# Optimization experiments

Hardware: AMD Instinct MI355X
Metric: run time of the kernel (lower is better)

The kernel has to match this reference:

```python
import jax, jax.numpy as jnp
import numpy as np

B, T, E, H = 2, 2048, 1024, 16
D = E // H  # head dim = 64
ROPE_BASE = 10000.0


def setup_inputs() -> dict:
    key = jax.random.key(0)
    k0, k1, k2 = jax.random.split(key, 3)
    s = 0.02  # GPT-style init scale
    return {
        "x": jax.random.normal(k0, (B, T, E), jnp.float32),
        "w_qkv": jax.random.normal(k1, (E, 3 * E), jnp.float32) * s,
        "b_qkv": jnp.zeros((3 * E,), jnp.float32),
        "w_out": jax.random.normal(k2, (E, E), jnp.float32) * s,
        "b_out": jnp.zeros((E,), jnp.float32),
    }


def _rope_tables(t, d, dtype):
    # Llama rotary with scale=1 (YaRN degenerates to vanilla RoPE)
    inv_freq = 1.0 / (ROPE_BASE ** (jnp.arange(0, d, 2, dtype=jnp.float32) / d))
    freqs = jnp.arange(t, dtype=jnp.float32)[:, None] * inv_freq[None, :]  # [T, D/2]
    emb = jnp.concatenate([freqs, freqs], axis=-1)  # [T, D]
    return jnp.cos(emb).astype(dtype), jnp.sin(emb).astype(dtype)


def _rotate_half(x):
    return jnp.concatenate([-x[..., D // 2:], x[..., : D // 2]], axis=-1)


def reference(x, w_qkv, b_qkv, w_out, b_out):
    # 1) fused QKV projection
    qkv = x @ w_qkv + b_qkv                      # [B, T, 3E]
    q, k, v = jnp.split(qkv, 3, axis=-1)

    def heads(t):
        return t.reshape(B, T, H, D).transpose(0, 2, 1, 3)  # [B, H, T, D]

    q, k, v = heads(q), heads(k), heads(v)

    # 2) rotary position embedding on q, k
    cos, sin = _rope_tables(T, D, x.dtype)       # [T, D], broadcasts over B, H
    q = q * cos + _rotate_half(q) * sin
    k = k * cos + _rotate_half(k) * sin

    # 3) causal scaled dot-product attention
    scale = jnp.asarray(1.0 / np.sqrt(D), x.dtype)
    scores = jnp.einsum("bhqd,bhkd->bhqk", q, k) * scale
    causal = jnp.tril(jnp.ones((T, T), dtype=bool))
    scores = jnp.where(causal, scores, jnp.finfo(scores.dtype).min)
    attn = jax.nn.softmax(scores, axis=-1)
    out = jnp.einsum("bhqk,bhkd->bhqd", attn, v)  # [B, H, T, D]

    # 4) merge heads + output projection
    out = out.transpose(0, 2, 1, 3).reshape(B, T, E)
    return out @ w_out + b_out
```

## Files before the change

kernel.cpp:

```cpp
#include <hip/hip_runtime.h>
#include <hip/hip_bf16.h>
#include <stdint.h>

#define B_  2
#define T_  2048
#define E_  1024
#define H_  16
#define D_  64
#define BH_ 32

typedef unsigned short ushort_t;
typedef __attribute__((ext_vector_type(8))) short bfrag;
typedef __attribute__((ext_vector_type(4))) short s16x4;
typedef __attribute__((ext_vector_type(4))) float f32x4;

__device__ __forceinline__ ushort_t f2b(float f) {
    uint32_t u = __builtin_bit_cast(uint32_t, f);
    u += 0x7fffu + ((u >> 16) & 1u);
    return (ushort_t)(u >> 16);
}
__device__ __forceinline__ float b2f(ushort_t h) {
    return __builtin_bit_cast(float, (uint32_t)h << 16);
}

#if defined(__has_builtin)
#if __has_builtin(__builtin_amdgcn_exp2f)
#define EXP2(x) __builtin_amdgcn_exp2f(x)
#endif
#endif
#ifndef EXP2
__device__ __forceinline__ float hexp2_(float x) {
    float r;
    asm volatile("v_exp_f32 %0, %1\n\ts_nop 1" : "=v"(r) : "v"(x));
    return r;
}
#define EXP2(x) hexp2_(x)
#endif

__device__ __forceinline__ uint32_t cvtpk_bf16(float lo, float hi) {
    uint32_t r;
    asm("v_cvt_pk_bf16_f32 %0, %1, %2" : "=v"(r) : "v"(lo), "v"(hi));
    return r;
}

typedef const __attribute__((address_space(1))) uint8_t* gas_t;
typedef __attribute__((address_space(3))) uint8_t* las_t;
__device__ __forceinline__ void gload_lds16(const void* g, void* l) {
    __builtin_amdgcn_global_load_lds((gas_t)g, (las_t)l, 16, 0, 0);
}

__global__ __launch_bounds__(256) void rope_table_kernel(float2* __restrict__ cs) {
    int id = blockIdx.x * 256 + threadIdx.x;
    int j = id & 31, t = id >> 5;
    float ang = (float)t * expf(-(float)j * 0.2878231366242558f);
    float s, c;
    sincosf(ang, &s, &c);
    cs[id] = make_float2(c, s);
}

__global__ __launch_bounds__(256) void cast_x_kernel(const float* __restrict__ in, ushort_t* __restrict__ out) {
    int i = (blockIdx.x * 256 + threadIdx.x) * 8;
    float4 a = *(const float4*)(in + i);
    float4 b = *(const float4*)(in + i + 4);
    ushort_t r[8] = {f2b(a.x), f2b(a.y), f2b(a.z), f2b(a.w), f2b(b.x), f2b(b.y), f2b(b.z), f2b(b.w)};
    *(uint4*)(out + i) = *(const uint4*)r;
}

__global__ __launch_bounds__(256) void transpose_cast_kernel(const float* __restrict__ in, ushort_t* __restrict__ out,
                                                             int R, int C) {
    __shared__ float tile[32][33];
    int tx = threadIdx.x, ty = threadIdx.y;
    int c0 = blockIdx.x * 32, r0 = blockIdx.y * 32;
#pragma unroll
    for (int i = 0; i < 4; ++i)
        tile[ty + i * 8][tx] = in[(size_t)(r0 + ty + i * 8) * C + c0 + tx];
    __syncthreads();
#pragma unroll
    for (int i = 0; i < 4; ++i)
        out[(size_t)(c0 + ty + i * 8) * R + r0 + tx] = f2b(tile[tx][ty + i * 8]);
}

__global__ __launch_bounds__(256) void gemm_qkv_kernel(const ushort_t* __restrict__ A, const ushort_t* __restrict__ Bt,
                                                       const float* __restrict__ bias, const float2* __restrict__ cstab,
                                                       ushort_t* __restrict__ qw, ushort_t* __restrict__ kw,
                                                       ushort_t* __restrict__ vw) {
    const int K = 1024;
    __shared__ ushort_t As[128 * 64];
    __shared__ ushort_t Bs[128 * 64];
    int tid = threadIdx.x, lane = tid & 63, wid = tid >> 6;
    int lm = lane & 15, lg = lane >> 4;
    int bid = blockIdx.x;
    int xcd = bid & 7, idx = bid >> 3;
    int bm = xcd * 4 + idx / 24;
    int bn = idx % 24;
    int wm = wid >> 1, wn = wid & 1;

    int cbase = bn * 128 + wn * 64;
    bool qk = (cbase < 2048);

    f32x4 acc[4][4] = {};
    const ushort_t* ag = A + (size_t)bm * 128 * K;
    const ushort_t* bg = Bt + (size_t)bn * 128 * K;

    for (int kt = 0; kt < K / 64; ++kt) {
        __syncthreads();
#pragma unroll
        for (int c = 0; c < 4; ++c) {
            int G = c * 256 + tid;
            int rr = G >> 3;
            int gs = (G & 7) ^ (rr & 7);
            gload_lds16(ag + (size_t)rr * K + kt * 64 + gs * 8, As + (c * 256 + wid * 64) * 8);
            gload_lds16(bg + (size_t)rr * K + kt * 64 + gs * 8, Bs + (c * 256 + wid * 64) * 8);
        }
        __syncthreads();
        bfrag a[2][4], b[2][4];
#pragma unroll
        for (int kk = 0; kk < 2; ++kk) {
#pragma unroll
            for (int mi = 0; mi < 4; ++mi) {
                int row = wm * 64 + mi * 16 + lm;
                int slot = (kk * 4 + lg) ^ (lm & 7);
                a[kk][mi] = *(const bfrag*)&As[row * 64 + slot * 8];
            }
#pragma unroll
            for (int ni = 0; ni < 4; ++ni) {
                int row = wn * 64 + ni * 16 + lm;
                int slot = (kk * 4 + lg) ^ (lm & 7);
                b[kk][ni] = *(const bfrag*)&Bs[row * 64 + slot * 8];
            }
        }
        if (qk) {
#pragma unroll
            for (int kk = 0; kk < 2; ++kk)
#pragma unroll
                for (int mi = 0; mi < 4; ++mi)
#pragma unroll
                    for (int ni = 0; ni < 4; ++ni)
                        acc[mi][ni] = __builtin_amdgcn_mfma_f32_16x16x32_bf16(b[kk][ni], a[kk][mi], acc[mi][ni], 0, 0, 0);
        } else {
#pragma unroll
            for (int kk = 0; kk < 2; ++kk)
#pragma unroll
                for (int mi = 0; mi < 4; ++mi)
#pragma unroll
                    for (int ni = 0; ni < 4; ++ni)
                        acc[mi][ni] = __builtin_amdgcn_mfma_f32_16x16x32_bf16(a[kk][mi], b[kk][ni], acc[mi][ni], 0, 0, 0);
        }
    }

    int sel = cbase >> 10;
    int h = (cbase & 1023) >> 6;
    if (qk) {
        ushort_t* dst = sel ? kw : qw;
        float scale = sel ? 1.0f : 0.18033688011112042f;
        float4 bias4[4];
#pragma unroll
        for (int ni = 0; ni < 4; ++ni)
            bias4[ni] = *(const float4*)&bias[cbase + ni * 16 + lg * 4];
#pragma unroll
        for (int mi = 0; mi < 4; ++mi) {
            int r = bm * 128 + wm * 64 + mi * 16 + lm;
            int bb = r >> 11, t = r & (T_ - 1);
            size_t rowbase = ((size_t)(bb * H_ + h) * T_ + t) * D_;
            const float4* csrow = (const float4*)(cstab + t * 32);
#pragma unroll
            for (int nip = 0; nip < 2; ++nip) {
                float4 ca = csrow[nip * 4 + lg];
                float4 cb = csrow[nip * 4 + lg + 2 * (nip == 0 ? 1 : 1) - 1];
                const float4* cs2 = (const float4*)(cstab + t * 32 + nip * 16 + lg * 4);
                ca = cs2[0]; cb = cs2[1];
                float xl[4], xh[4];
#pragma unroll
                for (int i = 0; i < 4; ++i) {
                    xl[i] = acc[mi][nip][i]     + ((const float*)&bias4[nip])[i];
                    xh[i] = acc[mi][nip + 2][i] + ((const float*)&bias4[nip + 2])[i];
                }
                float c0 = ca.x, s0 = ca.y, c1 = ca.z, s1 = ca.w;
                float c2 = cb.x, s2 = cb.y, c3 = cb.z, s3 = cb.w;
                float rl0 = (xl[0] * c0 - xh[0] * s0) * scale;
                float rl1 = (xl[1] * c1 - xh[1] * s1) * scale;
                float rl2 = (xl[2] * c2 - xh[2] * s2) * scale;
                float rl3 = (xl[3] * c3 - xh[3] * s3) * scale;
                float rh0 = (xh[0] * c0 + xl[0] * s0) * scale;
                float rh1 = (xh[1] * c1 + xl[1] * s1) * scale;
                float rh2 = (xh[2] * c2 + xl[2] * s2) * scale;
                float rh3 = (xh[3] * c3 + xl[3] * s3) * scale;
                uint2 wlo, whi;
                wlo.x = cvtpk_bf16(rl0, rl1); wlo.y = cvtpk_bf16(rl2, rl3);
                whi.x = cvtpk_bf16(rh0, rh1); whi.y = cvtpk_bf16(rh2, rh3);
                *(uint2*)&dst[rowbase + nip * 16 + lg * 4]      = wlo;
                *(uint2*)&dst[rowbase + 32 + nip * 16 + lg * 4] = whi;
            }
        }
    } else {
        float bb4[4];
#pragma unroll
        for (int ni = 0; ni < 4; ++ni) bb4[ni] = bias[cbase + ni * 16 + lm];
#pragma unroll
        for (int ni = 0; ni < 4; ++ni) {
            int d = ni * 16 + lm;
#pragma unroll
            for (int mi = 0; mi < 4; ++mi) {
                int r = bm * 128 + wm * 64 + mi * 16 + lg * 4;
                int bb = r >> 11, tq = r & (T_ - 1);
                uint2 w;
                w.x = cvtpk_bf16(acc[mi][ni][0] + bb4[ni], acc[mi][ni][1] + bb4[ni]);
                w.y = cvtpk_bf16(acc[mi][ni][2] + bb4[ni], acc[mi][ni][3] + bb4[ni]);
                *(uint2*)&vw[((size_t)(bb * H_ + h) * D_ + d) * T_ + tq] = w;
            }
        }
    }
}

__device__ __forceinline__ void stage_tile(const ushort_t* __restrict__ kb, const ushort_t* __restrict__ vb,
                                           ushort_t* kdst, ushort_t* vdst, int k0, int wid, int lane) {
#pragma unroll
    for (int c = 0; c < 2; ++c) {
        int G = (c * 4 + wid) * 64 + lane;
        int rr = G >> 3;
        int gs = (G & 7) ^ (rr & 7);
        gload_lds16(kb + (size_t)(k0 + rr) * D_ + gs * 8, kdst + (c * 4 + wid) * 512);
        gload_lds16(vb + (size_t)rr * T_ + k0 + gs * 8, vdst + (c * 4 + wid) * 512);
    }
}

__global__ __launch_bounds__(256, 2) void flash_kernel(const ushort_t* __restrict__ q, const ushort_t* __restrict__ k,
                                                       const ushort_t* __restrict__ vt, ushort_t* __restrict__ o) {
    __shared__ ushort_t smem[2][4096];
    int tid = threadIdx.x, lane = tid & 63, wid = tid >> 6;
    int lm = lane & 15, lg = lane >> 4;
    int x = blockIdx.x & 7, r = blockIdx.x >> 3;
    int half = r >> 5, idx = r & 31;
    int bh = x * 4 + (idx & 3);
    int jq = idx >> 2;
    int j = half ? jq : 15 - jq;
    int q0w = j * 128 + wid * 32;
    int b = bh >> 4, h = bh & 15;
    int nt = 2 * j + 2;

    const ushort_t* qb = q + (size_t)bh * T_ * D_;
    const ushort_t* kb = k + (size_t)bh * T_ * D_;
    const ushort_t* vb = vt + (size_t)bh * D_ * T_;

    bfrag aq[2][2];
#pragma unroll
    for (int s = 0; s < 2; ++s)
#pragma unroll
        for (int hh = 0; hh < 2; ++hh)
            aq[s][hh] = *(const bfrag*)(qb + (size_t)(q0w + s * 16 + lm) * D_ + hh * 32 + lg * 8);

    f32x4 acc[2][4] = {};
    float lsum[2] = {0.f, 0.f};

    for (int t = 0; t < nt; ++t) {
        int k0 = t * 64;
        __syncthreads();
        stage_tile(kb, vb, smem[0], smem[1], k0, wid, lane);
        asm volatile("s_waitcnt vmcnt(0)" ::: "memory");
        __builtin_amdgcn_sched_barrier(0);
        __syncthreads();

        if (k0 <= q0w + 31) {
            bfrag ka[4][2];
#pragma unroll
            for (int sb = 0; sb < 4; ++sb)
#pragma unroll
                for (int hh = 0; hh < 2; ++hh) {
                    int rr = sb * 16 + lm;
                    int gr = (hh * 4 + lg) ^ (rr & 7);
                    ka[sb][hh] = *(const bfrag*)&smem[0][rr * 64 + gr * 8];
                }
            s16x4 vq[4][4];
#pragma unroll
            for (int qq = 0; qq < 4; ++qq)
#pragma unroll
                for (int db = 0; db < 4; ++db) {
                    int rr = db * 16 + lm;
                    int gr = (qq * 2 + (lg >> 1)) ^ (rr & 7);
                    vq[qq][db] = *(const s16x4*)&smem[1][rr * 64 + gr * 8 + (lg & 1) * 4];
                }
            f32x4 st[2][4];
#pragma unroll
            for (int s = 0; s < 2; ++s)
#pragma unroll
                for (int sb = 0; sb < 4; ++sb) {
                    f32x4 z = {};
                    z = __builtin_amdgcn_mfma_f32_16x16x32_bf16(ka[sb][0], aq[s][0], z, 0, 0, 0);
                    st[s][sb] = __builtin_amdgcn_mfma_f32_16x16x32_bf16(ka[sb][1], aq[s][1], z, 0, 0, 0);
                }
            if (k0 + 63 > q0w) {
#pragma unroll
                for (int s = 0; s < 2; ++s)
#pragma unroll
                    for (int sb = 0; sb < 4; ++sb)
#pragma unroll
                        for (int i = 0; i < 4; ++i)
                            if (k0 + sb * 16 + lg * 4 + i > q0w + s * 16 + lm) st[s][sb][i] = -1e30f;
            }
#pragma unroll
            for (int s = 0; s < 2; ++s) {
                float pv[4][4];
#pragma unroll
                for (int sb = 0; sb < 4; ++sb)
#pragma unroll
                    for (int i = 0; i < 4; ++i)
                        pv[sb][i] = EXP2(st[s][sb][i]);
                lsum[s] += ((pv[0][0] + pv[0][1]) + (pv[0][2] + pv[0][3])) +
                           ((pv[1][0] + pv[1][1]) + (pv[1][2] + pv[1][3])) +
                           ((pv[2][0] + pv[2][1]) + (pv[2][2] + pv[2][3])) +
                           ((pv[3][0] + pv[3][1]) + (pv[3][2] + pv[3][3]));
                uint4 u0, u1;
                u0.x = cvtpk_bf16(pv[0][0], pv[0][1]);
                u0.y = cvtpk_bf16(pv[0][2], pv[0][3]);
                u0.z = cvtpk_bf16(pv[1][0], pv[1][1]);
                u0.w = cvtpk_bf16(pv[1][2], pv[1][3]);
                u1.x = cvtpk_bf16(pv[2][0], pv[2][1]);
                u1.y = cvtpk_bf16(pv[2][2], pv[2][3]);
                u1.z = cvtpk_bf16(pv[3][0], pv[3][1]);
                u1.w = cvtpk_bf16(pv[3][2], pv[3][3]);
                bfrag pf0 = __builtin_bit_cast(bfrag, u0);
                bfrag pf1 = __builtin_bit_cast(bfrag, u1);
#pragma unroll
                for (int db = 0; db < 4; ++db) {
                    bfrag va01 = __builtin_shufflevector(vq[0][db], vq[1][db], 0, 1, 2, 3, 4, 5, 6, 7);
                    bfrag va23 = __builtin_shufflevector(vq[2][db], vq[3][db], 0, 1, 2, 3, 4, 5, 6, 7);
                    acc[s][db] = __builtin_amdgcn_mfma_f32_16x16x32_bf16(va01, pf0, acc[s][db], 0, 0, 0);
                    acc[s][db] = __builtin_amdgcn_mfma_f32_16x16x32_bf16(va23, pf1, acc[s][db], 0, 0, 0);
                }
            }
        }
    }

#pragma unroll
    for (int s = 0; s < 2; ++s) {
        float lM = lsum[s];
        lM += __shfl_xor(lM, 16);
        lM += __shfl_xor(lM, 32);
        float inv = 1.0f / lM;
        int tq = q0w + s * 16 + lm;
        size_t ro = ((size_t)b * T_ + tq) * E_ + h * D_;
#pragma unroll
        for (int db = 0; db < 4; ++db) {
            uint2 w;
            w.x = cvtpk_bf16(acc[s][db][0] * inv, acc[s][db][1] * inv);
            w.y = cvtpk_bf16(acc[s][db][2] * inv, acc[s][db][3] * inv);
            *(uint2*)(o + ro + db * 16 + lg * 4) = w;
        }
    }
}

__global__ __launch_bounds__(256) void gemm_out_kernel(const ushort_t* __restrict__ A, const ushort_t* __restrict__ Bt,
                                                       const float* __restrict__ bias, float* __restrict__ out) {
    const int K = 1024;
    __shared__ ushort_t As[128 * 64];
    __shared__ ushort_t Bs[64 * 64];
    int tid = threadIdx.x, lane = tid & 63, wid = tid >> 6;
    int lm = lane & 15, lg = lane >> 4;
    int bid = blockIdx.x;
    int xcd = bid & 7, idx = bid >> 3;
    int bm = xcd * 4 + idx / 16;
    int bn = idx % 16;

    f32x4 acc[2][4] = {};
    const ushort_t* ag = A + (size_t)bm * 128 * K;
    const ushort_t* bg = Bt + (size_t)bn * 64 * K;

    for (int kt = 0; kt < K / 64; ++kt) {
        __syncthreads();
#pragma unroll
        for (int c = 0; c < 4; ++c) {
            int G = c * 256 + tid;
            int rr = G >> 3;
            int gs = (G & 7) ^ (rr & 7);
            gload_lds16(ag + (size_t)rr * K + kt * 64 + gs * 8, As + (c * 256 + wid * 64) * 8);
        }
#pragma unroll
        for (int c = 0; c < 2; ++c) {
            int G = c * 256 + tid;
            int rr = G >> 3;
            int gs = (G & 7) ^ (rr & 7);
            gload_lds16(bg + (size_t)rr * K + kt * 64 + gs * 8, Bs + (c * 256 + wid * 64) * 8);
        }
        __syncthreads();
        bfrag a[2][2], b[2][4];
#pragma unroll
        for (int kk = 0; kk < 2; ++kk) {
#pragma unroll
            for (int mi = 0; mi < 2; ++mi) {
                int row = wid * 32 + mi * 16 + lm;
                int slot = (kk * 4 + lg) ^ (lm & 7);
                a[kk][mi] = *(const bfrag*)&As[row * 64 + slot * 8];
            }
#pragma unroll
            for (int ni = 0; ni < 4; ++ni) {
                int row = ni * 16 + lm;
                int slot = (kk * 4 + lg) ^ (lm & 7);
                b[kk][ni] = *(const bfrag*)&Bs[row * 64 + slot * 8];
            }
        }
#pragma unroll
        for (int kk = 0; kk < 2; ++kk)
#pragma unroll
            for (int mi = 0; mi < 2; ++mi)
#pragma unroll
                for (int ni = 0; ni < 4; ++ni)
                    acc[mi][ni] = __builtin_amdgcn_mfma_f32_16x16x32_bf16(a[kk][mi], b[kk][ni], acc[mi][ni], 0, 0, 0);
    }
#pragma unroll
    for (int ni = 0; ni < 4; ++ni) {
        int c = bn * 64 + ni * 16 + lm;
        float bb = bias[c];
#pragma unroll
        for (int mi = 0; mi < 2; ++mi) {
#pragma unroll
            for (int i = 0; i < 4; ++i) {
                int r = bm * 128 + wid * 32 + mi * 16 + lg * 4 + i;
                out[(size_t)r * 1024 + c] = acc[mi][ni][i] + bb;
            }
        }
    }
}

extern "C" void kernel_launch(void* const* d_in, const int* in_sizes, int n_in,
                              void* d_out, int out_size, void* d_ws, size_t ws_size,
                              hipStream_t stream) {
    const float* x     = (const float*)d_in[0];
    const float* w_qkv = (const float*)d_in[1];
    const float* b_qkv = (const float*)d_in[2];
    const float* w_out = (const float*)d_in[3];
    const float* b_out = (const float*)d_in[4];
    float* out = (float*)d_out;

    ushort_t* ws    = (ushort_t*)d_ws;
    ushort_t* xb    = ws;
    ushort_t* wqkvT = xb + 4194304;
    ushort_t* woutT = wqkvT + 3145728;
    ushort_t* qw    = woutT + 1048576;
    ushort_t* kw    = qw + 4194304;
    ushort_t* vw    = kw + 4194304;
    ushort_t* ao    = vw + 4194304;
    float2*   cstab = (float2*)(ao + 4194304);

    rope_table_kernel<<<256, 256, 0, stream>>>(cstab);
    cast_x_kernel<<<2048, 256, 0, stream>>>(x, xb);
    transpose_cast_kernel<<<dim3(96, 32), dim3(32, 8), 0, stream>>>(w_qkv, wqkvT, 1024, 3072);
    transpose_cast_kernel<<<dim3(32, 32), dim3(32, 8), 0, stream>>>(w_out, woutT, 1024, 1024);
    gemm_qkv_kernel<<<dim3(768), 256, 0, stream>>>(xb, wqkvT, b_qkv, cstab, qw, kw, vw);
    flash_kernel<<<dim3(512), 256, 0, stream>>>(qw, kw, vw, ao);
    gemm_out_kernel<<<dim3(512), 256, 0, stream>>>(ao, woutT, b_out, out);
}
```

Before: 118.8 us.

## Double-buffer LDS in both GEMMs and merge prep kernels into one launch

Both the QKV and output-projection GEMMs now use two LDS buffers: the global-to-LDS load for the next K tile is issued before the MFMAs on the current tile, so load latency overlaps compute and each iteration has one barrier instead of two. The four preprocessing kernels (rope table, x cast, two weight transposes) are merged into one launch that dispatches on block index, removing three kernel launches. The cost is doubled LDS use per block (64KB for the QKV GEMM), which may lower occupancy, and the prep kernel is now a single block-heterogeneous grid. The RoPE epilogue gets a small cleanup of redundant loads.

```diff
diff --git a/kernel.cpp b/kernel.cpp
--- a/kernel.cpp
+++ b/kernel.cpp
@@ -18,9 +18,6 @@
     uint32_t u = __builtin_bit_cast(uint32_t, f);
     u += 0x7fffu + ((u >> 16) & 1u);
     return (ushort_t)(u >> 16);
-}
-__device__ __forceinline__ float b2f(ushort_t h) {
-    return __builtin_bit_cast(float, (uint32_t)h << 16);
 }
 
 #if defined(__has_builtin)
@@ -48,36 +45,46 @@
 __device__ __forceinline__ void gload_lds16(const void* g, void* l) {
     __builtin_amdgcn_global_load_lds((gas_t)g, (las_t)l, 16, 0, 0);
 }
-
-__global__ __launch_bounds__(256) void rope_table_kernel(float2* __restrict__ cs) {
-    int id = blockIdx.x * 256 + threadIdx.x;
-    int j = id & 31, t = id >> 5;
-    float ang = (float)t * expf(-(float)j * 0.2878231366242558f);
-    float s, c;
-    sincosf(ang, &s, &c);
-    cs[id] = make_float2(c, s);
-}
-
-__global__ __launch_bounds__(256) void cast_x_kernel(const float* __restrict__ in, ushort_t* __restrict__ out) {
-    int i = (blockIdx.x * 256 + threadIdx.x) * 8;
-    float4 a = *(const float4*)(in + i);
-    float4 b = *(const float4*)(in + i + 4);
-    ushort_t r[8] = {f2b(a.x), f2b(a.y), f2b(a.z), f2b(a.w), f2b(b.x), f2b(b.y), f2b(b.z), f2b(b.w)};
-    *(uint4*)(out + i) = *(const uint4*)r;
-}
-
-__global__ __launch_bounds__(256) void transpose_cast_kernel(const float* __restrict__ in, ushort_t* __restrict__ out,
-                                                             int R, int C) {
+__device__ __forceinline__ void drain_vmem() {
+    asm volatile("s_waitcnt vmcnt(0)" ::: "memory");
+    __builtin_amdgcn_sched_barrier(0);
+}
+
+__global__ __launch_bounds__(256) void prep_kernel(const float* __restrict__ x, const float* __restrict__ w_qkv,
+                                                   const float* __restrict__ w_out, ushort_t* __restrict__ xb,
+                                                   ushort_t* __restrict__ wqkvT, ushort_t* __restrict__ woutT,
+                                                   float2* __restrict__ cstab) {
     __shared__ float tile[32][33];
-    int tx = threadIdx.x, ty = threadIdx.y;
-    int c0 = blockIdx.x * 32, r0 = blockIdx.y * 32;
-#pragma unroll
-    for (int i = 0; i < 4; ++i)
-        tile[ty + i * 8][tx] = in[(size_t)(r0 + ty + i * 8) * C + c0 + tx];
-    __syncthreads();
-#pragma unroll
-    for (int i = 0; i < 4; ++i)
-        out[(size_t)(c0 + ty + i * 8) * R + r0 + tx] = f2b(tile[tx][ty + i * 8]);
+    int blk = blockIdx.x, tid = threadIdx.x;
+    if (blk < 256) {
+        int id = blk * 256 + tid;
+        int j = id & 31, t = id >> 5;
+        float ang = (float)t * expf(-(float)j * 0.2878231366242558f);
+        float s, c;
+        sincosf(ang, &s, &c);
+        cstab[id] = make_float2(c, s);
+    } else if (blk < 2304) {
+        int i = ((blk - 256) * 256 + tid) * 8;
+        float4 a = *(const float4*)(x + i);
+        float4 b = *(const float4*)(x + i + 4);
+        ushort_t r[8] = {f2b(a.x), f2b(a.y), f2b(a.z), f2b(a.w), f2b(b.x), f2b(b.y), f2b(b.z), f2b(b.w)};
+        *(uint4*)(xb + i) = *(const uint4*)r;
+    } else {
+        const float* in;
+        ushort_t* out;
+        int R, C, bx, by;
+        if (blk < 5376) { in = w_qkv; out = wqkvT; R = 1024; C = 3072; int t = blk - 2304; bx = t % 96; by = t / 96; }
+        else            { in = w_out; out = woutT; R = 1024; C = 1024; int t = blk - 5376; bx = t % 32; by = t / 32; }
+        int tx = tid & 31, ty = tid >> 5;
+        int c0 = bx * 32, r0 = by * 32;
+#pragma unroll
+        for (int i = 0; i < 4; ++i)
+            tile[ty + i * 8][tx] = in[(size_t)(r0 + ty + i * 8) * C + c0 + tx];
+        __syncthreads();
+#pragma unroll
+        for (int i = 0; i < 4; ++i)
+            out[(size_t)(c0 + ty + i * 8) * R + r0 + tx] = f2b(tile[tx][ty + i * 8]);
+    }
 }
 
 __global__ __launch_bounds__(256) void gemm_qkv_kernel(const ushort_t* __restrict__ A, const ushort_t* __restrict__ Bt,
@@ -85,8 +92,8 @@
                                                        ushort_t* __restrict__ qw, ushort_t* __restrict__ kw,
                                                        ushort_t* __restrict__ vw) {
     const int K = 1024;
-    __shared__ ushort_t As[128 * 64];
-    __shared__ ushort_t Bs[128 * 64];
+    __shared__ ushort_t As[2][128 * 64];
+    __shared__ ushort_t Bs[2][128 * 64];
     int tid = threadIdx.x, lane = tid & 63, wid = tid >> 6;
     int lm = lane & 15, lg = lane >> 4;
     int bid = blockIdx.x;
@@ -102,17 +109,23 @@
     const ushort_t* ag = A + (size_t)bm * 128 * K;
     const ushort_t* bg = Bt + (size_t)bn * 128 * K;
 
+#define QKV_STAGE(kt_, buf_)                                                              \
+    _Pragma("unroll")                                                                     \
+    for (int c = 0; c < 4; ++c) {                                                         \
+        int G = c * 256 + tid;                                                            \
+        int rr = G >> 3;                                                                  \
+        int gs = (G & 7) ^ (rr & 7);                                                      \
+        gload_lds16(ag + (size_t)rr * K + (kt_) * 64 + gs * 8, &As[buf_][(c * 256 + wid * 64) * 8]); \
+        gload_lds16(bg + (size_t)rr * K + (kt_) * 64 + gs * 8, &Bs[buf_][(c * 256 + wid * 64) * 8]); \
+    }
+
+    int cur = 0;
+    QKV_STAGE(0, 0);
+    drain_vmem();
+    __syncthreads();
+
     for (int kt = 0; kt < K / 64; ++kt) {
-        __syncthreads();
-#pragma unroll
-        for (int c = 0; c < 4; ++c) {
-            int G = c * 256 + tid;
-            int rr = G >> 3;
-            int gs = (G & 7) ^ (rr & 7);
-            gload_lds16(ag + (size_t)rr * K + kt * 64 + gs * 8, As + (c * 256 + wid * 64) * 8);
-            gload_lds16(bg + (size_t)rr * K + kt * 64 + gs * 8, Bs + (c * 256 + wid * 64) * 8);
-        }
-        __syncthreads();
+        if (kt + 1 < K / 64) { QKV_STAGE(kt + 1, cur ^ 1); }
         bfrag a[2][4], b[2][4];
 #pragma unroll
         for (int kk = 0; kk < 2; ++kk) {
@@ -120,13 +133,13 @@
             for (int mi = 0; mi < 4; ++mi) {
                 int row = wm * 64 + mi * 16 + lm;
                 int slot = (kk * 4 + lg) ^ (lm & 7);
-                a[kk][mi] = *(const bfrag*)&As[row * 64 + slot * 8];
+                a[kk][mi] = *(const bfrag*)&As[cur][row * 64 + slot * 8];
             }
 #pragma unroll
             for (int ni = 0; ni < 4; ++ni) {
                 int row = wn * 64 + ni * 16 + lm;
                 int slot = (kk * 4 + lg) ^ (lm & 7);
-                b[kk][ni] = *(const bfrag*)&Bs[row * 64 + slot * 8];
+                b[kk][ni] = *(const bfrag*)&Bs[cur][row * 64 + slot * 8];
             }
         }
         if (qk) {
@@ -146,7 +159,11 @@
                     for (int ni = 0; ni < 4; ++ni)
                         acc[mi][ni] = __builtin_amdgcn_mfma_f32_16x16x32_bf16(a[kk][mi], b[kk][ni], acc[mi][ni], 0, 0, 0);
         }
-    }
+        drain_vmem();
+        __syncthreads();
+        cur ^= 1;
+    }
+#undef QKV_STAGE
 
     int sel = cbase >> 10;
     int h = (cbase & 1023) >> 6;
@@ -162,29 +179,24 @@
             int r = bm * 128 + wm * 64 + mi * 16 + lm;
             int bb = r >> 11, t = r & (T_ - 1);
             size_t rowbase = ((size_t)(bb * H_ + h) * T_ + t) * D_;
-            const float4* csrow = (const float4*)(cstab + t * 32);
 #pragma unroll
             for (int nip = 0; nip < 2; ++nip) {
-                float4 ca = csrow[nip * 4 + lg];
-                float4 cb = csrow[nip * 4 + lg + 2 * (nip == 0 ? 1 : 1) - 1];
                 const float4* cs2 = (const float4*)(cstab + t * 32 + nip * 16 + lg * 4);
-                ca = cs2[0]; cb = cs2[1];
+                float4 ca = cs2[0], cb = cs2[1];
                 float xl[4], xh[4];
 #pragma unroll
                 for (int i = 0; i < 4; ++i) {
                     xl[i] = acc[mi][nip][i]     + ((const float*)&bias4[nip])[i];
                     xh[i] = acc[mi][nip + 2][i] + ((const float*)&bias4[nip + 2])[i];
                 }
-                float c0 = ca.x, s0 = ca.y, c1 = ca.z, s1 = ca.w;
-                float c2 = cb.x, s2 = cb.y, c3 = cb.z, s3 = cb.w;
-                float rl0 = (xl[0] * c0 - xh[0] * s0) * scale;
-                float rl1 = (xl[1] * c1 - xh[1] * s1) * scale;
-                float rl2 = (xl[2] * c2 - xh[2] * s2) * scale;
-                float rl3 = (xl[3] * c3 - xh[3] * s3) * scale;
-                float rh0 = (xh[0] * c0 + xl[0] * s0) * scale;
-                float rh1 = (xh[1] * c1 + xl[1] * s1) * scale;
-                float rh2 = (xh[2] * c2 + xl[2] * s2) * scale;
-                float rh3 = (xh[3] * c3 + xl[3] * s3) * scale;
+                float rl0 = (xl[0] * ca.x - xh[0] * ca.y) * scale;
+                float rl1 = (xl[1] * ca.z - xh[1] * ca.w) * scale;
+                float rl2 = (xl[2] * cb.x - xh[2] * cb.y) * scale;
+                float rl3 = (xl[3] * cb.z - xh[3] * cb.w) * scale;
+                float rh0 = (xh[0] * ca.x + xl[0] * ca.y) * scale;
+                float rh1 = (xh[1] * ca.z + xl[1] * ca.w) * scale;
+                float rh2 = (xh[2] * cb.x + xl[2] * cb.y) * scale;
+                float rh3 = (xh[3] * cb.z + xl[3] * cb.w) * scale;
                 uint2 wlo, whi;
                 wlo.x = cvtpk_bf16(rl0, rl1); wlo.y = cvtpk_bf16(rl2, rl3);
                 whi.x = cvtpk_bf16(rh0, rh1); whi.y = cvtpk_bf16(rh2, rh3);
@@ -256,8 +268,7 @@
         int k0 = t * 64;
         __syncthreads();
         stage_tile(kb, vb, smem[0], smem[1], k0, wid, lane);
-        asm volatile("s_waitcnt vmcnt(0)" ::: "memory");
-        __builtin_amdgcn_sched_barrier(0);
+        drain_vmem();
         __syncthreads();
 
         if (k0 <= q0w + 31) {
@@ -352,8 +363,8 @@
 __global__ __launch_bounds__(256) void gemm_out_kernel(const ushort_t* __restrict__ A, const ushort_t* __restrict__ Bt,
                                                        const float* __restrict__ bias, float* __restrict__ out) {
     const int K = 1024;
-    __shared__ ushort_t As[128 * 64];
-    __shared__ ushort_t Bs[64 * 64];
+    __shared__ ushort_t As[2][128 * 64];
+    __shared__ ushort_t Bs[2][64 * 64];
     int tid = threadIdx.x, lane = tid & 63, wid = tid >> 6;
     int lm = lane & 15, lg = lane >> 4;
     int bid = blockIdx.x;
@@ -365,23 +376,29 @@
     const ushort_t* ag = A + (size_t)bm * 128 * K;
     const ushort_t* bg = Bt + (size_t)bn * 64 * K;
 
+#define OUT_STAGE(kt_, buf_)                                                              \
+    _Pragma("unroll")                                                                     \
+    for (int c = 0; c < 4; ++c) {                                                         \
+        int G = c * 256 + tid;                                                            \
+        int rr = G >> 3;                                                                  \
+        int gs = (G & 7) ^ (rr & 7);                                                      \
+        gload_lds16(ag + (size_t)rr * K + (kt_) * 64 + gs * 8, &As[buf_][(c * 256 + wid * 64) * 8]); \
+    }                                                                                     \
+    _Pragma("unroll")                                                                     \
+    for (int c = 0; c < 2; ++c) {                                                         \
+        int G = c * 256 + tid;                                                            \
+        int rr = G >> 3;                                                                  \
+        int gs = (G & 7) ^ (rr & 7);                                                      \
+        gload_lds16(bg + (size_t)rr * K + (kt_) * 64 + gs * 8, &Bs[buf_][(c * 256 + wid * 64) * 8]); \
+    }
+
+    int cur = 0;
+    OUT_STAGE(0, 0);
+    drain_vmem();
+    __syncthreads();
+
     for (int kt = 0; kt < K / 64; ++kt) {
-        __syncthreads();
-#pragma unroll
-        for (int c = 0; c < 4; ++c) {
-            int G = c * 256 + tid;
-            int rr = G >> 3;
-            int gs = (G & 7) ^ (rr & 7);
-            gload_lds16(ag + (size_t)rr * K + kt * 64 + gs * 8, As + (c * 256 + wid * 64) * 8);
-        }
-#pragma unroll
-        for (int c = 0; c < 2; ++c) {
-            int G = c * 256 + tid;
-            int rr = G >> 3;
-            int gs = (G & 7) ^ (rr & 7);
-            gload_lds16(bg + (size_t)rr * K + kt * 64 + gs * 8, Bs + (c * 256 + wid * 64) * 8);
-        }
-        __syncthreads();
+        if (kt + 1 < K / 64) { OUT_STAGE(kt + 1, cur ^ 1); }
         bfrag a[2][2], b[2][4];
 #pragma unroll
         for (int kk = 0; kk < 2; ++kk) {
@@ -389,13 +406,13 @@
             for (int mi = 0; mi < 2; ++mi) {
                 int row = wid * 32 + mi * 16 + lm;
                 int slot = (kk * 4 + lg) ^ (lm & 7);
-                a[kk][mi] = *(const bfrag*)&As[row * 64 + slot * 8];
+                a[kk][mi] = *(const bfrag*)&As[cur][row * 64 + slot * 8];
             }
 #pragma unroll
             for (int ni = 0; ni < 4; ++ni) {
                 int row = ni * 16 + lm;
                 int slot = (kk * 4 + lg) ^ (lm & 7);
-                b[kk][ni] = *(const bfrag*)&Bs[row * 64 + slot * 8];
+                b[kk][ni] = *(const bfrag*)&Bs[cur][row * 64 + slot * 8];
             }
         }
 #pragma unroll
@@ -405,7 +422,12 @@
 #pragma unroll
                 for (int ni = 0; ni < 4; ++ni)
                     acc[mi][ni] = __builtin_amdgcn_mfma_f32_16x16x32_bf16(a[kk][mi], b[kk][ni], acc[mi][ni], 0, 0, 0);
-    }
+        drain_vmem();
+        __syncthreads();
+        cur ^= 1;
+    }
+#undef OUT_STAGE
+
 #pragma unroll
     for (int ni = 0; ni < 4; ++ni) {
         int c = bn * 64 + ni * 16 + lm;
@@ -441,10 +463,7 @@
     ushort_t* ao    = vw + 4194304;
     float2*   cstab = (float2*)(ao + 4194304);
 
-    rope_table_kernel<<<256, 256, 0, stream>>>(cstab);
-    cast_x_kernel<<<2048, 256, 0, stream>>>(x, xb);
-    transpose_cast_kernel<<<dim3(96, 32), dim3(32, 8), 0, stream>>>(w_qkv, wqkvT, 1024, 3072);
-    transpose_cast_kernel<<<dim3(32, 32), dim3(32, 8), 0, stream>>>(w_out, woutT, 1024, 1024);
+    prep_kernel<<<dim3(6400), 256, 0, stream>>>(x, w_qkv, w_out, xb, wqkvT, woutT, cstab);
     gemm_qkv_kernel<<<dim3(768), 256, 0, stream>>>(xb, wqkvT, b_qkv, cstab, qw, kw, vw);
     flash_kernel<<<dim3(512), 256, 0, stream>>>(qw, kw, vw, ao);
     gemm_out_kernel<<<dim3(512), 256, 0, stream>>>(ao, woutT, b_out, out);
```

Measured after the change: 113.2 us. 4.7% less time.
